# Kernel tuning notes

Hardware: AMD Instinct MI355X
Metric: run time of the kernel (lower is better)

Reference implementation:

```python
import jax, jax.numpy as jnp
import numpy as np

B, Q, T, H, V = 8, 1, 2048, 512, 32000


def setup_inputs() -> dict:
    key = jax.random.key(0)
    k0, k1, k2, k3, k4 = jax.random.split(key, 5)
    s1 = 1.0 / np.sqrt(2 * H)
    return {
        "input_embeds": jax.random.normal(k0, (B, Q, H), dtype=jnp.float32),
        "target_embeds": jax.random.normal(k1, (B, T, H), dtype=jnp.float32),
        "input_mask": jnp.ones((B, T), dtype=jnp.float32),
        # MLP params: l1 Linear(2H->H, bias), l2 Linear(H->1, no bias)
        "w1": (jax.random.normal(k2, (H, 2 * H), dtype=jnp.float32) * s1),
        "b1": jnp.zeros((H,), dtype=jnp.float32),
        "w2": (jax.random.normal(k3, (H,), dtype=jnp.float32) * (1.0 / np.sqrt(H))),
        # decoder: Linear(H->V, no bias) -> weight [V, H]
        "decoder_weight": (jax.random.normal(k4, (V, H), dtype=jnp.float32) * 0.02),
    }


def reference(input_embeds, target_embeds, input_mask, w1, b1, w2, decoder_weight):
    h = w1.shape[0]
    # l1(cat(q, t)) == q @ W1q^T + t @ W1t^T + b1  (split first linear)
    w1q, w1t = w1[:, :h], w1[:, h:]
    q_proj = jnp.einsum('bqh,kh->bqk', input_embeds, w1q)        # [B,Q,H]
    t_proj = jnp.einsum('bth,kh->btk', target_embeds, w1t)       # [B,T,H]
    # pairwise query x target MLP scoring
    ht = jax.nn.relu(q_proj[:, :, None, :] + t_proj[:, None, :, :] + b1)  # [B,Q,T,H]
    repair_logits = jnp.einsum('bqtk,k->bqt', ht, w2)             # [B,Q,T]
    # _mask: mask*logits - 1000*(1-mask); mask [B,T] -> [B,1,T]
    mask = input_mask[:, None, :]
    repair_logits = mask * repair_logits - 1000.0 * (1.0 - mask)
    # decoder branch: query x vocab-row MLP scoring
    d_proj = jnp.einsum('vh,kh->vk', decoder_weight, w1t)         # [V,H]
    hd = jax.nn.relu(q_proj[:, :, None, :] + d_proj[None, None, :, :] + b1)  # [B,Q,V,H]
    decoder_logits = jnp.einsum('bqvk,k->bqv', hd, w2)            # [B,Q,V]
    out = jnp.concatenate([decoder_logits, repair_logits], axis=2)  # [B,Q,V+T]
    return jnp.squeeze(out, axis=1)  # Q == 1 -> [B, V+T]
```

## Files before the change

kernel.cpp:

```cpp
#include <hip/hip_runtime.h>
#include <hip/hip_bf16.h>

#define Hdim 512
#define Bdim 8
#define Tdim 2048
#define Vdim 32000
#define OUTW (Vdim + Tdim)
#define DEC_TILES (Vdim / 128)
#define REP_TILES ((Bdim * Tdim) / 128)
#define NTILES (DEC_TILES + REP_TILES)

typedef __attribute__((ext_vector_type(8))) short short8;
typedef __attribute__((ext_vector_type(16))) float f32x16;

__device__ __forceinline__ unsigned packbf2(float a, float b) {
    __hip_bfloat162 h = __float22bfloat162_rn(make_float2(a, b));
    union { __hip_bfloat162 h; unsigned u; } c; c.h = h;
    return c.u;
}

union U8 { unsigned u[4]; short8 s; };
__device__ __forceinline__ short8 cvt8(const float4 f0, const float4 f1) {
    U8 r;
    r.u[0] = packbf2(f0.x, f0.y); r.u[1] = packbf2(f0.z, f0.w);
    r.u[2] = packbf2(f1.x, f1.y); r.u[3] = packbf2(f1.z, f1.w);
    return r.s;
}

#define WT_BLOCKS 128
#define QP_BLOCKS (Bdim * Hdim / 4)

__global__ __launch_bounds__(256) void prep_kernel(
    const float* __restrict__ w1, const float* __restrict__ x,
    const float* __restrict__ b1,
    unsigned short* __restrict__ wt, float* __restrict__ qp)
{
    const int bid = blockIdx.x;
    if (bid < WT_BLOCKS) {
        const int i = bid * 256 + threadIdx.x;
        const int n = i >> 6;
        const int kk = (i & 63) * 8;
        const float4* s = (const float4*)(w1 + (size_t)n * 1024 + 512 + kk);
        const float4 v0 = s[0], v1 = s[1];
        uint4 o;
        o.x = packbf2(v0.x, v0.y); o.y = packbf2(v0.z, v0.w);
        o.z = packbf2(v1.x, v1.y); o.w = packbf2(v1.z, v1.w);
        ((uint4*)wt)[i] = o;
    } else {
        const int widx = (bid - WT_BLOCKS) * 4 + (threadIdx.x >> 6);
        const int lane = threadIdx.x & 63;
        const int b = widx >> 9, k = widx & 511;
        const float4* xr = (const float4*)(x + b * Hdim);
        const float4* wr = (const float4*)(w1 + (size_t)k * 1024);
        float4 x0 = xr[lane * 2], x1 = xr[lane * 2 + 1];
        float4 w0 = wr[lane * 2], w1v = wr[lane * 2 + 1];
        float s = x0.x * w0.x + x0.y * w0.y + x0.z * w0.z + x0.w * w0.w
                + x1.x * w1v.x + x1.y * w1v.y + x1.z * w1v.z + x1.w * w1v.w;
#pragma unroll
        for (int off = 32; off > 0; off >>= 1) s += __shfl_down(s, off);
        if (lane == 0) qp[b * Hdim + k] = s + b1[k];
    }
}

__global__ __launch_bounds__(256, 3) void gemm_kernel(
    const float* __restrict__ Adec,
    const float* __restrict__ Atgt,
    const unsigned short* __restrict__ Wt,
    const float* __restrict__ qp,
    const float* __restrict__ w2,
    float* __restrict__ Pd,
    float* __restrict__ Pr)
{
    __shared__ union {
        struct { float A[128][64]; unsigned short W[128][64]; } g;
        struct { float qT[8][128]; float w2c[128]; } e;
    } u;

    const int tid  = threadIdx.x;
    const int lane = tid & 63;
    const int w    = tid >> 6;

    const int b = blockIdx.x;
    const int mt = (b >> 5) * 8 + (b & 7);
    if (mt >= NTILES) return;
    const int chunk = (b >> 3) & 3;
    const int n0 = chunk << 7;
    const bool is_dec = (mt < DEC_TILES);
    const int m0 = (is_dec ? mt : mt - DEC_TILES) << 7;
    const float* __restrict__ Af = is_dec ? Adec : Atgt;

    const int arow = w * 4 + (lane >> 4);
    const int achk = (lane & 15) ^ arow;
    const float* gA = Af + (size_t)(m0 + arow) * 512 + achk * 4;

    const int sr = lane >> 3;
    const int sc = (lane & 7) ^ sr;
    const unsigned short* gW = Wt + (size_t)(n0 + w * 32 + sr) * 512 + sc * 8;

    f32x16 acc00, acc01, acc10, acc11;
#pragma unroll
    for (int i = 0; i < 16; ++i) { acc00[i] = 0.f; acc01[i] = 0.f; acc10[i] = 0.f; acc11[i] = 0.f; }

    const int wm  = (w & 1) << 6;
    const int wn  = (w >> 1) << 6;
    const int l31 = lane & 31;
    const int kh  = lane >> 5;
    const int rx7  = l31 & 7;
    const int rx15 = l31 & 15;

    for (int h0 = 0; h0 < Hdim; h0 += 64) {
        __syncthreads();
#pragma unroll
        for (int j = 0; j < 8; ++j)
            __builtin_amdgcn_global_load_lds(
                (const __attribute__((address_space(1))) unsigned int*)(gA + j * 16 * 512),
                (__attribute__((address_space(3))) unsigned int*)(&u.g.A[j * 16 + w * 4][0]),
                16, 0, 0);
#pragma unroll
        for (int j = 0; j < 4; ++j)
            __builtin_amdgcn_global_load_lds(
                (const __attribute__((address_space(1))) unsigned int*)(gW + j * 8 * 512),
                (__attribute__((address_space(3))) unsigned int*)(&u.g.W[w * 32 + j * 8][0]),
                16, 0, 0);
        gA += 64; gW += 64;
        __syncthreads();
#pragma unroll
        for (int s = 0; s < 4; ++s) {
            const int g  = s * 2 + kh;
            const int p0 = ((2 * g) ^ rx15) << 2;
            const int p1 = ((2 * g + 1) ^ rx15) << 2;
            const float4 a0f0 = *(const float4*)&u.g.A[wm + l31][p0];
            const float4 a0f1 = *(const float4*)&u.g.A[wm + l31][p1];
            const float4 a1f0 = *(const float4*)&u.g.A[wm + l31 + 32][p0];
            const float4 a1f1 = *(const float4*)&u.g.A[wm + l31 + 32][p1];
            const short8 a0 = cvt8(a0f0, a0f1);
            const short8 a1 = cvt8(a1f0, a1f1);
            const int ow = ((g ^ rx7) << 3);
            const short8 b0 = *(const short8*)&u.g.W[wn + l31][ow];
            const short8 b1 = *(const short8*)&u.g.W[wn + l31 + 32][ow];
            acc00 = __builtin_amdgcn_mfma_f32_32x32x16_bf16(b0, a0, acc00, 0, 0, 0);
            acc01 = __builtin_amdgcn_mfma_f32_32x32x16_bf16(b0, a1, acc01, 0, 0, 0);
            acc10 = __builtin_amdgcn_mfma_f32_32x32x16_bf16(b1, a0, acc10, 0, 0, 0);
            acc11 = __builtin_amdgcn_mfma_f32_32x32x16_bf16(b1, a1, acc11, 0, 0, 0);
        }
    }

    __syncthreads();
    {
        const int qb = tid >> 5;
        const int qn = (tid & 31) << 2;
        *(float4*)&u.e.qT[qb][qn] = *(const float4*)&qp[qb * Hdim + n0 + qn];
        if (tid < 32) *(float4*)&u.e.w2c[tid << 2] = *(const float4*)&w2[n0 + (tid << 2)];
    }
    __syncthreads();

    const int kh4 = kh << 2;
    const int slice = (chunk << 1) + (wn >> 6);

    float4 wvA[4], wvB[4];
#pragma unroll
    for (int run = 0; run < 4; ++run) {
        wvA[run] = *(const float4*)&u.e.w2c[wn + run * 8 + kh4];
        wvB[run] = *(const float4*)&u.e.w2c[wn + 32 + run * 8 + kh4];
    }

#define EPI_PAIR(QROW, T0, T1) do {                                          \
        float _p0 = 0.f, _p1 = 0.f;                                          \
        _Pragma("unroll")                                                    \
        for (int run = 0; run < 4; ++run) {                                  \
            const float4 q0 = *(const float4*)((QROW) + wn + run * 8 + kh4); \
            const float4 q1 = *(const float4*)((QROW) + wn + 32 + run * 8 + kh4); \
            const float4 wA = wvA[run], wB = wvB[run];                       \
            _p0 += fmaxf(acc00[run * 4 + 0] + q0.x, 0.f) * wA.x;             \
            _p1 += fmaxf(acc01[run * 4 + 0] + q0.x, 0.f) * wA.x;             \
            _p0 += fmaxf(acc10[run * 4 + 0] + q1.x, 0.f) * wB.x;             \
            _p1 += fmaxf(acc11[run * 4 + 0] + q1.x, 0.f) * wB.x;             \
            _p0 += fmaxf(acc00[run * 4 + 1] + q0.y, 0.f) * wA.y;             \
            _p1 += fmaxf(acc01[run * 4 + 1] + q0.y, 0.f) * wA.y;             \
            _p0 += fmaxf(acc10[run * 4 + 1] + q1.y, 0.f) * wB.y;             \
            _p1 += fmaxf(acc11[run * 4 + 1] + q1.y, 0.f) * wB.y;             \
            _p0 += fmaxf(acc00[run * 4 + 2] + q0.z, 0.f) * wA.z;             \
            _p1 += fmaxf(acc01[run * 4 + 2] + q0.z, 0.f) * wA.z;             \
            _p0 += fmaxf(acc10[run * 4 + 2] + q1.z, 0.f) * wB.z;             \
            _p1 += fmaxf(acc11[run * 4 + 2] + q1.z, 0.f) * wB.z;             \
            _p0 += fmaxf(acc00[run * 4 + 3] + q0.w, 0.f) * wA.w;             \
            _p1 += fmaxf(acc01[run * 4 + 3] + q0.w, 0.f) * wA.w;             \
            _p0 += fmaxf(acc10[run * 4 + 3] + q1.w, 0.f) * wB.w;             \
            _p1 += fmaxf(acc11[run * 4 + 3] + q1.w, 0.f) * wB.w;             \
        }                                                                    \
        T0 = _p0 + __shfl_xor(_p0, 32);                                      \
        T1 = _p1 + __shfl_xor(_p1, 32);                                      \
    } while (0)

    if (is_dec) {
#pragma unroll
        for (int b2 = 0; b2 < 8; ++b2) {
            float t0, t1;
            EPI_PAIR(&u.e.qT[b2][0], t0, t1);
            if (kh == 0) {
                float* o = Pd + ((size_t)slice * 8 + b2) * Vdim + m0 + wm;
                o[l31]      = t0;
                o[32 + l31] = t1;
            }
        }
    } else {
        const int bfix = m0 >> 11;
        float t0, t1;
        EPI_PAIR(&u.e.qT[bfix][0], t0, t1);
        if (kh == 0) {
            float* o = Pr + (size_t)slice * (Bdim * Tdim) + m0 + wm;
            o[l31]      = t0;
            o[32 + l31] = t1;
        }
    }
#undef EPI_PAIR
}

#define RED_DEC_BLOCKS (Bdim * Vdim / 4 / 256)
#define RED_REP_BLOCKS (Bdim * Tdim / 4 / 256)

__global__ __launch_bounds__(256) void reduce_kernel(
    const float* __restrict__ Pd, const float* __restrict__ Pr,
    const float* __restrict__ mask, float* __restrict__ out)
{
    const int blk = blockIdx.x;
    if (blk < RED_DEC_BLOCKS) {
        const int i4 = blk * 256 + threadIdx.x;
        const int b  = i4 / (Vdim / 4);
        const int v4 = i4 - b * (Vdim / 4);
        const float4* p = (const float4*)Pd + (size_t)b * (Vdim / 4) + v4;
        const size_t cs = (size_t)Bdim * (Vdim / 4);
        float4 s = p[0];
#pragma unroll
        for (int c = 1; c < 8; ++c) {
            const float4 v = p[c * cs];
            s.x += v.x; s.y += v.y; s.z += v.z; s.w += v.w;
        }
        *(float4*)(out + (size_t)b * OUTW + v4 * 4) = s;
    } else {
        const int i4 = (blk - RED_DEC_BLOCKS) * 256 + threadIdx.x;
        const int rr = i4 * 4;
        const int b  = rr >> 11;
        const int t  = rr & 2047;
        const float4* p = (const float4*)Pr + i4;
        const size_t cs = (size_t)(Bdim * Tdim / 4);
        float4 s = p[0];
#pragma unroll
        for (int c = 1; c < 8; ++c) {
            const float4 v = p[c * cs];
            s.x += v.x; s.y += v.y; s.z += v.z; s.w += v.w;
        }
        const float4 mv = *(const float4*)(mask + b * Tdim + t);
        float4 o;
        o.x = mv.x * s.x - 1000.f * (1.f - mv.x);
        o.y = mv.y * s.y - 1000.f * (1.f - mv.y);
        o.z = mv.z * s.z - 1000.f * (1.f - mv.z);
        o.w = mv.w * s.w - 1000.f * (1.f - mv.w);
        *(float4*)(out + (size_t)b * OUTW + Vdim + t) = o;
    }
}

extern "C" void kernel_launch(void* const* d_in, const int* in_sizes, int n_in,
                              void* d_out, int out_size, void* d_ws, size_t ws_size,
                              hipStream_t stream) {
    const float* input_embeds  = (const float*)d_in[0];
    const float* target_embeds = (const float*)d_in[1];
    const float* input_mask    = (const float*)d_in[2];
    const float* w1            = (const float*)d_in[3];
    const float* b1            = (const float*)d_in[4];
    const float* w2            = (const float*)d_in[5];
    const float* decoder_w     = (const float*)d_in[6];
    float* out = (float*)d_out;

    float* qp = (float*)d_ws;
    unsigned short* wt = (unsigned short*)((char*)d_ws + 16384);
    float* Pd = (float*)((char*)d_ws + 16384 + 524288);
    float* Pr = Pd + (size_t)8 * Bdim * Vdim;

    prep_kernel<<<WT_BLOCKS + QP_BLOCKS, 256, 0, stream>>>(w1, input_embeds, b1, wt, qp);
    gemm_kernel<<<48 * 32, 256, 0, stream>>>(
        decoder_w, target_embeds, wt, qp, w2, Pd, Pr);
    reduce_kernel<<<RED_DEC_BLOCKS + RED_REP_BLOCKS, 256, 0, stream>>>(
        Pd, Pr, input_mask, out);
}
```

Before: 192.0 us.

## Double-buffer GEMM K-loop with async LDS prefetch at half K-step

The GEMM main loop now uses two LDS buffers with a K-step of 32 instead of one buffer with K-step 64. Each iteration issues the global-to-LDS loads for the next step before computing on the current one, so memory latency can overlap with MFMA work, and it needs only one barrier per step. The LDS layout is changed to pack the 128-row tile into two 64-column halves with new swizzled addressing, keeping the shared footprint the same. The cost is twice as many loop iterations with less work in each, plus more complex index math. The loads into the next buffer also have no explicit wait before that buffer is read, so correctness depends on how the barrier drains outstanding loads.

```diff
diff --git a/kernel.cpp b/kernel.cpp
--- a/kernel.cpp
+++ b/kernel.cpp
@@ -72,7 +72,7 @@
     float* __restrict__ Pr)
 {
     __shared__ union {
-        struct { float A[128][64]; unsigned short W[128][64]; } g;
+        struct { float A[2][64][64]; unsigned short W[2][64][64]; } g;
         struct { float qT[8][128]; float w2c[128]; } e;
     } u;
 
@@ -89,13 +89,37 @@
     const int m0 = (is_dec ? mt : mt - DEC_TILES) << 7;
     const float* __restrict__ Af = is_dec ? Adec : Atgt;
 
-    const int arow = w * 4 + (lane >> 4);
-    const int achk = (lane & 15) ^ arow;
-    const float* gA = Af + (size_t)(m0 + arow) * 512 + achk * 4;
-
-    const int sr = lane >> 3;
-    const int sc = (lane & 7) ^ sr;
-    const unsigned short* gW = Wt + (size_t)(n0 + w * 32 + sr) * 512 + sc * 8;
+    const float* gAp[4];
+#pragma unroll
+    for (int j = 0; j < 4; ++j) {
+        const int rr = w * 16 + j * 4 + (lane >> 4);
+        const int lc = (lane & 15) ^ (rr & 15);
+        gAp[j] = Af + (size_t)(m0 + rr + 64 * (lc >> 3)) * 512 + (lc & 7) * 4;
+    }
+    const unsigned short* gWp[2];
+    {
+        const int lcw = (lane & 7) ^ (lane >> 3);
+#pragma unroll
+        for (int j = 0; j < 2; ++j) {
+            const int rr = w * 16 + j * 8 + (lane >> 3);
+            gWp[j] = Wt + (size_t)(n0 + rr + 64 * (lcw >> 2)) * 512 + (lcw & 3) * 8;
+        }
+    }
+
+#define STAGE(bb, koff) do {                                                  \
+        _Pragma("unroll")                                                     \
+        for (int j = 0; j < 4; ++j)                                           \
+            __builtin_amdgcn_global_load_lds(                                 \
+                (const __attribute__((address_space(1))) unsigned int*)(gAp[j] + (koff)), \
+                (__attribute__((address_space(3))) unsigned int*)(&u.g.A[bb][w * 16 + j * 4][0]), \
+                16, 0, 0);                                                    \
+        _Pragma("unroll")                                                     \
+        for (int j = 0; j < 2; ++j)                                           \
+            __builtin_amdgcn_global_load_lds(                                 \
+                (const __attribute__((address_space(1))) unsigned int*)(gWp[j] + (koff)), \
+                (__attribute__((address_space(3))) unsigned int*)(&u.g.W[bb][w * 16 + j * 8][0]), \
+                16, 0, 0);                                                    \
+    } while (0)
 
     f32x16 acc00, acc01, acc10, acc11;
 #pragma unroll
@@ -105,47 +129,43 @@
     const int wn  = (w >> 1) << 6;
     const int l31 = lane & 31;
     const int kh  = lane >> 5;
+    const int rx15 = l31 & 15;
     const int rx7  = l31 & 7;
-    const int rx15 = l31 & 15;
-
-    for (int h0 = 0; h0 < Hdim; h0 += 64) {
-        __syncthreads();
-#pragma unroll
-        for (int j = 0; j < 8; ++j)
-            __builtin_amdgcn_global_load_lds(
-                (const __attribute__((address_space(1))) unsigned int*)(gA + j * 16 * 512),
-                (__attribute__((address_space(3))) unsigned int*)(&u.g.A[j * 16 + w * 4][0]),
-                16, 0, 0);
-#pragma unroll
-        for (int j = 0; j < 4; ++j)
-            __builtin_amdgcn_global_load_lds(
-                (const __attribute__((address_space(1))) unsigned int*)(gW + j * 8 * 512),
-                (__attribute__((address_space(3))) unsigned int*)(&u.g.W[w * 32 + j * 8][0]),
-                16, 0, 0);
-        gA += 64; gW += 64;
-        __syncthreads();
-#pragma unroll
-        for (int s = 0; s < 4; ++s) {
+    const int ha  = wm >> 6;
+    const int hw  = wn >> 6;
+
+    STAGE(0, 0);
+    __syncthreads();
+
+    int cur = 0;
+    for (int t = 0; t < 16; ++t) {
+        if (t < 15) STAGE(cur ^ 1, (t + 1) * 32);
+        const float (* __restrict__ Ab)[64] = u.g.A[cur];
+        const unsigned short (* __restrict__ Wb)[64] = u.g.W[cur];
+#pragma unroll
+        for (int s = 0; s < 2; ++s) {
             const int g  = s * 2 + kh;
-            const int p0 = ((2 * g) ^ rx15) << 2;
-            const int p1 = ((2 * g + 1) ^ rx15) << 2;
-            const float4 a0f0 = *(const float4*)&u.g.A[wm + l31][p0];
-            const float4 a0f1 = *(const float4*)&u.g.A[wm + l31][p1];
-            const float4 a1f0 = *(const float4*)&u.g.A[wm + l31 + 32][p0];
-            const float4 a1f1 = *(const float4*)&u.g.A[wm + l31 + 32][p1];
+            const int p0 = ((ha * 8 + 2 * g) ^ rx15) << 2;
+            const int p1 = ((ha * 8 + 2 * g + 1) ^ rx15) << 2;
+            const float4 a0f0 = *(const float4*)&Ab[l31][p0];
+            const float4 a0f1 = *(const float4*)&Ab[l31][p1];
+            const float4 a1f0 = *(const float4*)&Ab[l31 + 32][p0];
+            const float4 a1f1 = *(const float4*)&Ab[l31 + 32][p1];
             const short8 a0 = cvt8(a0f0, a0f1);
             const short8 a1 = cvt8(a1f0, a1f1);
-            const int ow = ((g ^ rx7) << 3);
-            const short8 b0 = *(const short8*)&u.g.W[wn + l31][ow];
-            const short8 b1 = *(const short8*)&u.g.W[wn + l31 + 32][ow];
+            const int ow = ((hw * 4 + g) ^ rx7) << 3;
+            const short8 b0 = *(const short8*)&Wb[l31][ow];
+            const short8 b1 = *(const short8*)&Wb[l31 + 32][ow];
             acc00 = __builtin_amdgcn_mfma_f32_32x32x16_bf16(b0, a0, acc00, 0, 0, 0);
             acc01 = __builtin_amdgcn_mfma_f32_32x32x16_bf16(b0, a1, acc01, 0, 0, 0);
             acc10 = __builtin_amdgcn_mfma_f32_32x32x16_bf16(b1, a0, acc10, 0, 0, 0);
             acc11 = __builtin_amdgcn_mfma_f32_32x32x16_bf16(b1, a1, acc11, 0, 0, 0);
         }
-    }
-
-    __syncthreads();
+        __syncthreads();
+        cur ^= 1;
+    }
+#undef STAGE
+
     {
         const int qb = tid >> 5;
         const int qn = (tid & 31) << 2;
```

After: 176.2 us. 1.09x faster.

## Double-buffer GEMM with register prefetch and bf16 LDS tiles

Applied to the files above, without the earlier changes.

Replaces the direct global-to-LDS fp32 A loads with register-staged global loads that are converted to bf16 before being written to LDS. The K loop becomes a two-buffer pipeline with 32-wide K steps, so the next tile's global loads overlap the current MFMA compute and only one barrier is needed per step. The smaller LDS footprint lets the launch bounds rise to 4 blocks per SM. This adds register pressure and uses hand-placed waitcnt and barrier instructions, which risks ordering mistakes and spills under the tighter occupancy bound.

```diff
diff --git a/kernel.cpp b/kernel.cpp
--- a/kernel.cpp
+++ b/kernel.cpp
@@ -62,7 +62,7 @@
     }
 }
 
-__global__ __launch_bounds__(256, 3) void gemm_kernel(
+__global__ __launch_bounds__(256, 4) void gemm_kernel(
     const float* __restrict__ Adec,
     const float* __restrict__ Atgt,
     const unsigned short* __restrict__ Wt,
@@ -72,7 +72,7 @@
     float* __restrict__ Pr)
 {
     __shared__ union {
-        struct { float A[128][64]; unsigned short W[128][64]; } g;
+        struct { unsigned short A[2][64][64]; unsigned short W[2][64][64]; } g;
         struct { float qT[8][128]; float w2c[128]; } e;
     } u;
 
@@ -89,13 +89,37 @@
     const int m0 = (is_dec ? mt : mt - DEC_TILES) << 7;
     const float* __restrict__ Af = is_dec ? Adec : Atgt;
 
-    const int arow = w * 4 + (lane >> 4);
-    const int achk = (lane & 15) ^ arow;
-    const float* gA = Af + (size_t)(m0 + arow) * 512 + achk * 4;
-
-    const int sr = lane >> 3;
-    const int sc = (lane & 7) ^ sr;
-    const unsigned short* gW = Wt + (size_t)(n0 + w * 32 + sr) * 512 + sc * 8;
+    const int sr2 = tid >> 1;
+    const int sh  = tid & 1;
+    const float* gAq = Af + (size_t)(m0 + sr2) * 512 + sh * 16;
+    const short* gWq = (const short*)Wt + (size_t)(n0 + sr2) * 512 + sh * 16;
+    const int wrr = sr2 & 63;
+    const int wsb = ((sr2 >> 6) << 2) + (sh << 1);
+    const int wp0 = ((wsb)     ^ (wrr & 7)) << 3;
+    const int wp1 = ((wsb + 1) ^ (wrr & 7)) << 3;
+
+    float4 rA0, rA1, rA2, rA3;
+    short8 rW0, rW1;
+
+#define GLOAD() do {                                                          \
+        rA0 = *(const float4*)(gAq);      rA1 = *(const float4*)(gAq + 4);    \
+        rA2 = *(const float4*)(gAq + 8);  rA3 = *(const float4*)(gAq + 12);   \
+        rW0 = *(const short8*)(gWq);      rW1 = *(const short8*)(gWq + 8);    \
+        gAq += 32; gWq += 32;                                                 \
+    } while (0)
+
+#define CVT_WRITE(bb) do {                                                    \
+        *(short8*)&u.g.A[bb][wrr][wp0] = cvt8(rA0, rA1);                      \
+        *(short8*)&u.g.A[bb][wrr][wp1] = cvt8(rA2, rA3);                      \
+        *(short8*)&u.g.W[bb][wrr][wp0] = rW0;                                 \
+        *(short8*)&u.g.W[bb][wrr][wp1] = rW1;                                 \
+    } while (0)
+
+#define BAR_LK() do {                                                         \
+        asm volatile("s_waitcnt lgkmcnt(0)" ::: "memory");                    \
+        __builtin_amdgcn_s_barrier();                                         \
+        __builtin_amdgcn_sched_barrier(0);                                    \
+    } while (0)
 
     f32x16 acc00, acc01, acc10, acc11;
 #pragma unroll
@@ -105,47 +129,48 @@
     const int wn  = (w >> 1) << 6;
     const int l31 = lane & 31;
     const int kh  = lane >> 5;
-    const int rx7  = l31 & 7;
-    const int rx15 = l31 & 15;
-
-    for (int h0 = 0; h0 < Hdim; h0 += 64) {
-        __syncthreads();
-#pragma unroll
-        for (int j = 0; j < 8; ++j)
-            __builtin_amdgcn_global_load_lds(
-                (const __attribute__((address_space(1))) unsigned int*)(gA + j * 16 * 512),
-                (__attribute__((address_space(3))) unsigned int*)(&u.g.A[j * 16 + w * 4][0]),
-                16, 0, 0);
-#pragma unroll
-        for (int j = 0; j < 4; ++j)
-            __builtin_amdgcn_global_load_lds(
-                (const __attribute__((address_space(1))) unsigned int*)(gW + j * 8 * 512),
-                (__attribute__((address_space(3))) unsigned int*)(&u.g.W[w * 32 + j * 8][0]),
-                16, 0, 0);
-        gA += 64; gW += 64;
-        __syncthreads();
-#pragma unroll
-        for (int s = 0; s < 4; ++s) {
-            const int g  = s * 2 + kh;
-            const int p0 = ((2 * g) ^ rx15) << 2;
-            const int p1 = ((2 * g + 1) ^ rx15) << 2;
-            const float4 a0f0 = *(const float4*)&u.g.A[wm + l31][p0];
-            const float4 a0f1 = *(const float4*)&u.g.A[wm + l31][p1];
-            const float4 a1f0 = *(const float4*)&u.g.A[wm + l31 + 32][p0];
-            const float4 a1f1 = *(const float4*)&u.g.A[wm + l31 + 32][p1];
-            const short8 a0 = cvt8(a0f0, a0f1);
-            const short8 a1 = cvt8(a1f0, a1f1);
-            const int ow = ((g ^ rx7) << 3);
-            const short8 b0 = *(const short8*)&u.g.W[wn + l31][ow];
-            const short8 b1 = *(const short8*)&u.g.W[wn + l31 + 32][ow];
-            acc00 = __builtin_amdgcn_mfma_f32_32x32x16_bf16(b0, a0, acc00, 0, 0, 0);
-            acc01 = __builtin_amdgcn_mfma_f32_32x32x16_bf16(b0, a1, acc01, 0, 0, 0);
-            acc10 = __builtin_amdgcn_mfma_f32_32x32x16_bf16(b1, a0, acc10, 0, 0, 0);
-            acc11 = __builtin_amdgcn_mfma_f32_32x32x16_bf16(b1, a1, acc11, 0, 0, 0);
-        }
-    }
-
-    __syncthreads();
+    const int rx7 = l31 & 7;
+    const int ha  = wm >> 6;
+    const int hw  = wn >> 6;
+
+#define COMPUTE(bb) do {                                                      \
+        _Pragma("unroll")                                                     \
+        for (int s = 0; s < 2; ++s) {                                         \
+            const int g  = s * 2 + kh;                                        \
+            const int soA = (((ha << 2) + g) ^ rx7) << 3;                     \
+            const int soW = (((hw << 2) + g) ^ rx7) << 3;                     \
+            const short8 a0 = *(const short8*)&u.g.A[bb][l31][soA];           \
+            const short8 a1 = *(const short8*)&u.g.A[bb][l31 + 32][soA];      \
+            const short8 b0 = *(const short8*)&u.g.W[bb][l31][soW];           \
+            const short8 b1 = *(const short8*)&u.g.W[bb][l31 + 32][soW];      \
+            acc00 = __builtin_amdgcn_mfma_f32_32x32x16_bf16(b0, a0, acc00, 0, 0, 0); \
+            acc01 = __builtin_amdgcn_mfma_f32_32x32x16_bf16(b0, a1, acc01, 0, 0, 0); \
+            acc10 = __builtin_amdgcn_mfma_f32_32x32x16_bf16(b1, a0, acc10, 0, 0, 0); \
+            acc11 = __builtin_amdgcn_mfma_f32_32x32x16_bf16(b1, a1, acc11, 0, 0, 0); \
+        }                                                                     \
+    } while (0)
+
+    GLOAD();
+    CVT_WRITE(0);
+    GLOAD();
+    BAR_LK();
+
+    int cur = 0;
+    for (int t = 0; t < 16; ++t) {
+        COMPUTE(cur);
+        if (t < 15) {
+            CVT_WRITE(cur ^ 1);
+            if (t < 14) GLOAD();
+        }
+        BAR_LK();
+        cur ^= 1;
+    }
+
+#undef COMPUTE
+#undef GLOAD
+#undef CVT_WRITE
+#undef BAR_LK
+
     {
         const int qb = tid >> 5;
         const int qn = (tid & 31) << 2;
```

After: 189.1 us. About the same (-1.5%).
